# Kernel tuning notes

Measured on AMD Instinct MI355X. Metric: run time of the kernel, lower is better.

Reference implementation:

```python
import jax, jax.numpy as jnp
import numpy as np
import math

B, H, S, D = 2, 8, 2048, 64

def setup_inputs() -> dict:
    key = jax.random.key(0)
    kq, kk, kv, km = jax.random.split(key, 4)
    q = jax.random.normal(kq, (B, H, S, D), dtype=jnp.float32)
    k = jax.random.normal(kk, (B, H, S, D), dtype=jnp.float32)
    v = jax.random.normal(kv, (B, H, S, D), dtype=jnp.float32)
    mask = jax.random.randint(km, (B, S, S), 0, 2, dtype=jnp.int32)
    return {"q": q, "k": k, "v": v, "mask": mask}

def reference(q, k, v, mask):
    # NOTE: faithful to the torch module's quirks:
    #   d = k.size(1) -> scale by sqrt(n_heads), not sqrt(head_dim)
    #   softmax over dim=1 (the HEAD axis), not the key axis
    d = k.shape[1]
    # [B,H,S,S]
    att_score = jnp.einsum('bhqd,bhkd->bhqk', q, k) / math.sqrt(d)
    m = mask[:, None, :, :]  # unsqueeze(1) -> [B,1,S,S]
    att_score = jnp.where(m == 0, jnp.float32(-1e11), att_score)
    att_score = jax.nn.softmax(att_score, axis=1)  # softmax over head dim (quirk)
    # dropout is identity in eval mode
    z = jnp.einsum('bhqk,bhkd->bhqd', att_score, v)
    return (z, att_score)
```

## Files before the change

### kernel.cpp

```cpp
#include <hip/hip_runtime.h>
#include <hip/hip_bf16.h>
#include <cmath>

#define B_ 2
#define H_ 8
#define S_ 2048
#define D_ 64
#define TQ 16
#define TK 32
#define KCHUNKS 8
#define TPC ((S_ / TK) / KCHUNKS)

typedef __bf16 bf16x8 __attribute__((ext_vector_type(8)));
typedef float  f32x4  __attribute__((ext_vector_type(4)));

#define SB_STRIDE 33
#define AB_STRIDE 40


__global__ __launch_bounds__(256, 4)
void attn_fused(const float* __restrict__ qg, const float* __restrict__ kg,
                const float* __restrict__ vg, const int* __restrict__ maskg,
                float* __restrict__ zout, float* __restrict__ attout)
{
    __shared__ float  sbuf[H_][TQ][SB_STRIDE];
    __shared__ __bf16 abuf[H_][TQ][AB_STRIDE];

    const int tid  = threadIdx.x;
    const int lane = tid & 63;
    const int wave = tid >> 6;
    const int n16  = lane & 15;
    const int quad = lane >> 4;

    const int bi    = blockIdx.x;
    const int b     = bi & 1;
    const int qt    = (bi >> 1) & 127;
    const int chunk = bi >> 8;
    const int q0    = qt * TQ;

    const float scale = 0.35355339059327373f;

    bf16x8 qhi[2][2], qlo[2][2];
    #pragma unroll
    for (int hh = 0; hh < 2; ++hh) {
        const int h = wave * 2 + hh;
        const float* qp = qg + (size_t)((b * H_ + h) * S_ + q0 + n16) * D_;
        #pragma unroll
        for (int kk = 0; kk < 2; ++kk) {
            const float4* p = (const float4*)(qp + kk * 32 + quad * 8);
            float4 f0 = p[0], f1 = p[1];
            float fv[8] = {f0.x, f0.y, f0.z, f0.w, f1.x, f1.y, f1.z, f1.w};
            bf16x8 hi, lo;
            #pragma unroll
            for (int j = 0; j < 8; ++j) {
                float fs = fv[j] * scale;
                __bf16 h16 = (__bf16)fs;
                hi[j] = h16;
                lo[j] = (__bf16)(fs - (float)h16);
            }
            qhi[hh][kk] = hi; qlo[hh][kk] = lo;
        }
    }

    f32x4 acc[2][4];
    #pragma unroll
    for (int hh = 0; hh < 2; ++hh)
        #pragma unroll
        for (int d = 0; d < 4; ++d)
            acc[hh][d] = (f32x4){0.f, 0.f, 0.f, 0.f};

    for (int kt = 0; kt < TPC; ++kt) {
        const int k0 = chunk * (TK * TPC) + kt * TK;

        #pragma unroll
        for (int hh = 0; hh < 2; ++hh) {
            const int h = wave * 2 + hh;
            #pragma unroll
            for (int ks = 0; ks < 2; ++ks) {
                f32x4 c = (f32x4){0.f, 0.f, 0.f, 0.f};
                #pragma unroll
                for (int kk = 0; kk < 2; ++kk) {
                    const float* kp = kg + (size_t)((b * H_ + h) * S_ + k0 + ks * 16 + n16) * D_
                                      + kk * 32 + quad * 8;
                    float4 f0 = ((const float4*)kp)[0], f1 = ((const float4*)kp)[1];
                    float fv[8] = {f0.x, f0.y, f0.z, f0.w, f1.x, f1.y, f1.z, f1.w};
                    bf16x8 khi, klo;
                    #pragma unroll
                    for (int j = 0; j < 8; ++j) {
                        __bf16 h16 = (__bf16)fv[j];
                        khi[j] = h16;
                        klo[j] = (__bf16)(fv[j] - (float)h16);
                    }
                    c = __builtin_amdgcn_mfma_f32_16x16x32_bf16(qhi[hh][kk], khi, c, 0, 0, 0);
                    c = __builtin_amdgcn_mfma_f32_16x16x32_bf16(qlo[hh][kk], khi, c, 0, 0, 0);
                    c = __builtin_amdgcn_mfma_f32_16x16x32_bf16(qhi[hh][kk], klo, c, 0, 0, 0);
                }
                #pragma unroll
                for (int r = 0; r < 4; ++r)
                    sbuf[h][quad * 4 + r][ks * 16 + n16] = c[r];
            }
        }
        __syncthreads();

        #pragma unroll
        for (int rep = 0; rep < 2; ++rep) {
            const int pos = tid + rep * 256;
            const int qq  = pos >> 5;
            const int kk2 = pos & 31;
            const int msk = maskg[(size_t)(b * S_ + q0 + qq) * S_ + k0 + kk2];
            float sv[8];
            float mx = -INFINITY;
            #pragma unroll
            for (int h = 0; h < H_; ++h) { sv[h] = sbuf[h][qq][kk2]; mx = fmaxf(mx, sv[h]); }
            float sum = 0.f;
            #pragma unroll
            for (int h = 0; h < H_; ++h) { sv[h] = __expf(sv[h] - mx); sum += sv[h]; }
            const float inv = 1.0f / sum;
            #pragma unroll
            for (int h = 0; h < H_; ++h) {
                const float a = (msk == 0) ? 0.125f : sv[h] * inv;
                attout[(size_t)((b * H_ + h) * S_ + q0 + qq) * S_ + k0 + kk2] = a;
                abuf[h][qq][kk2] = (__bf16)a;
            }
        }
        __syncthreads();

        #pragma unroll
        for (int hh = 0; hh < 2; ++hh) {
            const int h = wave * 2 + hh;
            bf16x8 af = *(const bf16x8*)&abuf[h][n16][quad * 8];
            #pragma unroll
            for (int dsb = 0; dsb < 4; ++dsb) {
                const float* vp = vg + (size_t)((b * H_ + h) * S_ + k0 + quad * 8) * D_
                                  + dsb * 16 + n16;
                bf16x8 bf;
                #pragma unroll
                for (int j = 0; j < 8; ++j)
                    bf[j] = (__bf16)vp[(size_t)j * D_];
                acc[hh][dsb] = __builtin_amdgcn_mfma_f32_16x16x32_bf16(af, bf, acc[hh][dsb], 0, 0, 0);
            }
        }
    }

    #pragma unroll
    for (int hh = 0; hh < 2; ++hh) {
        const int h = wave * 2 + hh;
        #pragma unroll
        for (int dsb = 0; dsb < 4; ++dsb)
            #pragma unroll
            for (int r = 0; r < 4; ++r)
                atomicAdd(&zout[(size_t)((b * H_ + h) * S_ + q0 + quad * 4 + r) * D_
                                + dsb * 16 + n16],
                          acc[hh][dsb][r]);
    }
}

extern "C" void kernel_launch(void* const* d_in, const int* in_sizes, int n_in,
                              void* d_out, int out_size, void* d_ws, size_t ws_size,
                              hipStream_t stream) {
    const float* q    = (const float*)d_in[0];
    const float* k    = (const float*)d_in[1];
    const float* v    = (const float*)d_in[2];
    const int*   mask = (const int*)d_in[3];
    float* z   = (float*)d_out;
    float* att = (float*)d_out + (size_t)B_ * H_ * S_ * D_;

    hipMemsetAsync(z, 0, (size_t)B_ * H_ * S_ * D_ * sizeof(float), stream);

    attn_fused<<<dim3(KCHUNKS * B_ * (S_ / TQ)), dim3(256), 0, stream>>>(q, k, v, mask, z, att);
}
```

Measured before the change: 532.5 us.

## Precompute bf16 hi/lo K split and transposed bf16 V in prep kernels

Adds two preprocessing kernels. One splits K into bf16 hi/lo arrays once, so the main kernel no longer redoes the split for every query tile. The other writes V transposed in bf16, so the PV MFMA operand loads become one contiguous 16-byte read per lane instead of eight strided fp32 loads. The softmax phase now handles two keys per thread with vectorized mask, score, attention-output and abuf accesses, and the sbuf stride changes to match. This costs two extra launches and workspace traffic.

```diff
diff --git a/kernel.cpp b/kernel.cpp
--- a/kernel.cpp
+++ b/kernel.cpp
@@ -14,13 +14,66 @@
 typedef __bf16 bf16x8 __attribute__((ext_vector_type(8)));
 typedef float  f32x4  __attribute__((ext_vector_type(4)));
 
-#define SB_STRIDE 33
+#define SB_STRIDE 42
 #define AB_STRIDE 40
 
+#define NK ((size_t)B_ * H_ * S_ * D_)
+
+__global__ __launch_bounds__(256)
+void prep_k(const float* __restrict__ kg, __bf16* __restrict__ khi, __bf16* __restrict__ klo)
+{
+    const size_t i = ((size_t)blockIdx.x * 256 + threadIdx.x) * 8;
+    float4 f0 = ((const float4*)(kg + i))[0];
+    float4 f1 = ((const float4*)(kg + i))[1];
+    float fv[8] = {f0.x, f0.y, f0.z, f0.w, f1.x, f1.y, f1.z, f1.w};
+    bf16x8 hi, lo;
+    #pragma unroll
+    for (int j = 0; j < 8; ++j) {
+        __bf16 h = (__bf16)fv[j];
+        hi[j] = h;
+        lo[j] = (__bf16)(fv[j] - (float)h);
+    }
+    *(bf16x8*)(khi + i) = hi;
+    *(bf16x8*)(klo + i) = lo;
+}
+
+__global__ __launch_bounds__(256)
+void prep_vt(const float* __restrict__ vg, __bf16* __restrict__ vt)
+{
+    __shared__ float tile[64][65];
+    const int bh = blockIdx.x >> 5;
+    const int kt = blockIdx.x & 31;
+    const int t  = threadIdx.x;
+    {
+        const int key = t >> 2, seg = t & 3;
+        const float* src = vg + ((size_t)bh * S_ + kt * 64 + key) * D_ + seg * 16;
+        #pragma unroll
+        for (int i = 0; i < 4; ++i) {
+            float4 f = ((const float4*)src)[i];
+            tile[key][seg * 16 + i * 4 + 0] = f.x;
+            tile[key][seg * 16 + i * 4 + 1] = f.y;
+            tile[key][seg * 16 + i * 4 + 2] = f.z;
+            tile[key][seg * 16 + i * 4 + 3] = f.w;
+        }
+    }
+    __syncthreads();
+    {
+        const int d = t >> 2, seg = t & 3;
+        bf16x8 o0, o1;
+        #pragma unroll
+        for (int j = 0; j < 8; ++j) o0[j] = (__bf16)tile[seg * 16 + j][d];
+        #pragma unroll
+        for (int j = 0; j < 8; ++j) o1[j] = (__bf16)tile[seg * 16 + 8 + j][d];
+        __bf16* dst = vt + ((size_t)bh * D_ + d) * S_ + kt * 64 + seg * 16;
+        *(bf16x8*)dst       = o0;
+        *((bf16x8*)dst + 1) = o1;
+    }
+}
 
 __global__ __launch_bounds__(256, 4)
-void attn_fused(const float* __restrict__ qg, const float* __restrict__ kg,
-                const float* __restrict__ vg, const int* __restrict__ maskg,
+void attn_fused(const float* __restrict__ qg,
+                const __bf16* __restrict__ khi_g, const __bf16* __restrict__ klo_g,
+                const __bf16* __restrict__ vt_g,  const int* __restrict__ maskg,
                 float* __restrict__ zout, float* __restrict__ attout)
 {
     __shared__ float  sbuf[H_][TQ][SB_STRIDE];
@@ -69,6 +122,9 @@
         for (int d = 0; d < 4; ++d)
             acc[hh][d] = (f32x4){0.f, 0.f, 0.f, 0.f};
 
+    const int sqq = tid >> 4;
+    const int skp = (tid & 15) * 2;
+
     for (int kt = 0; kt < TPC; ++kt) {
         const int k0 = chunk * (TK * TPC) + kt * TK;
 
@@ -77,20 +133,13 @@
             const int h = wave * 2 + hh;
             #pragma unroll
             for (int ks = 0; ks < 2; ++ks) {
+                const size_t krow = ((size_t)(b * H_ + h) * S_ + k0 + ks * 16 + n16) * D_
+                                    + quad * 8;
                 f32x4 c = (f32x4){0.f, 0.f, 0.f, 0.f};
                 #pragma unroll
                 for (int kk = 0; kk < 2; ++kk) {
-                    const float* kp = kg + (size_t)((b * H_ + h) * S_ + k0 + ks * 16 + n16) * D_
-                                      + kk * 32 + quad * 8;
-                    float4 f0 = ((const float4*)kp)[0], f1 = ((const float4*)kp)[1];
-                    float fv[8] = {f0.x, f0.y, f0.z, f0.w, f1.x, f1.y, f1.z, f1.w};
-                    bf16x8 khi, klo;
-                    #pragma unroll
-                    for (int j = 0; j < 8; ++j) {
-                        __bf16 h16 = (__bf16)fv[j];
-                        khi[j] = h16;
-                        klo[j] = (__bf16)(fv[j] - (float)h16);
-                    }
+                    bf16x8 khi = *(const bf16x8*)(khi_g + krow + kk * 32);
+                    bf16x8 klo = *(const bf16x8*)(klo_g + krow + kk * 32);
                     c = __builtin_amdgcn_mfma_f32_16x16x32_bf16(qhi[hh][kk], khi, c, 0, 0, 0);
                     c = __builtin_amdgcn_mfma_f32_16x16x32_bf16(qlo[hh][kk], khi, c, 0, 0, 0);
                     c = __builtin_amdgcn_mfma_f32_16x16x32_bf16(qhi[hh][kk], klo, c, 0, 0, 0);
@@ -102,25 +151,32 @@
         }
         __syncthreads();
 
-        #pragma unroll
-        for (int rep = 0; rep < 2; ++rep) {
-            const int pos = tid + rep * 256;
-            const int qq  = pos >> 5;
-            const int kk2 = pos & 31;
-            const int msk = maskg[(size_t)(b * S_ + q0 + qq) * S_ + k0 + kk2];
-            float sv[8];
-            float mx = -INFINITY;
-            #pragma unroll
-            for (int h = 0; h < H_; ++h) { sv[h] = sbuf[h][qq][kk2]; mx = fmaxf(mx, sv[h]); }
-            float sum = 0.f;
-            #pragma unroll
-            for (int h = 0; h < H_; ++h) { sv[h] = __expf(sv[h] - mx); sum += sv[h]; }
-            const float inv = 1.0f / sum;
+        {
+            const int2 m2 = *(const int2*)&maskg[(size_t)(b * S_ + q0 + sqq) * S_ + k0 + skp];
+            float2 sv[8];
+            float mx0 = -INFINITY, mx1 = -INFINITY;
             #pragma unroll
             for (int h = 0; h < H_; ++h) {
-                const float a = (msk == 0) ? 0.125f : sv[h] * inv;
-                attout[(size_t)((b * H_ + h) * S_ + q0 + qq) * S_ + k0 + kk2] = a;
-                abuf[h][qq][kk2] = (__bf16)a;
+                float2 s = *(const float2*)&sbuf[h][sqq][skp];
+                sv[h] = s;
+                mx0 = fmaxf(mx0, s.x); mx1 = fmaxf(mx1, s.y);
+            }
+            float sum0 = 0.f, sum1 = 0.f;
+            #pragma unroll
+            for (int h = 0; h < H_; ++h) {
+                sv[h].x = __expf(sv[h].x - mx0); sum0 += sv[h].x;
+                sv[h].y = __expf(sv[h].y - mx1); sum1 += sv[h].y;
+            }
+            const float inv0 = 1.0f / sum0, inv1 = 1.0f / sum1;
+            #pragma unroll
+            for (int h = 0; h < H_; ++h) {
+                const float a0 = (m2.x == 0) ? 0.125f : sv[h].x * inv0;
+                const float a1 = (m2.y == 0) ? 0.125f : sv[h].y * inv1;
+                *(float2*)&attout[(size_t)((b * H_ + h) * S_ + q0 + sqq) * S_ + k0 + skp]
+                    = make_float2(a0, a1);
+                union { __bf16 bh2[2]; unsigned u; } pk;
+                pk.bh2[0] = (__bf16)a0; pk.bh2[1] = (__bf16)a1;
+                *(unsigned*)&abuf[h][sqq][skp] = pk.u;
             }
         }
         __syncthreads();
@@ -131,12 +187,8 @@
             bf16x8 af = *(const bf16x8*)&abuf[h][n16][quad * 8];
             #pragma unroll
             for (int dsb = 0; dsb < 4; ++dsb) {
-                const float* vp = vg + (size_t)((b * H_ + h) * S_ + k0 + quad * 8) * D_
-                                  + dsb * 16 + n16;
-                bf16x8 bf;
-                #pragma unroll
-                for (int j = 0; j < 8; ++j)
-                    bf[j] = (__bf16)vp[(size_t)j * D_];
+                bf16x8 bf = *(const bf16x8*)(vt_g
+                    + ((size_t)(b * H_ + h) * D_ + dsb * 16 + n16) * S_ + k0 + quad * 8);
                 acc[hh][dsb] = __builtin_amdgcn_mfma_f32_16x16x32_bf16(af, bf, acc[hh][dsb], 0, 0, 0);
             }
         }
@@ -163,9 +215,17 @@
     const float* v    = (const float*)d_in[2];
     const int*   mask = (const int*)d_in[3];
     float* z   = (float*)d_out;
-    float* att = (float*)d_out + (size_t)B_ * H_ * S_ * D_;
-
-    hipMemsetAsync(z, 0, (size_t)B_ * H_ * S_ * D_ * sizeof(float), stream);
-
-    attn_fused<<<dim3(KCHUNKS * B_ * (S_ / TQ)), dim3(256), 0, stream>>>(q, k, v, mask, z, att);
-}
+    float* att = (float*)d_out + NK;
+
+    __bf16* khi = (__bf16*)d_ws;
+    __bf16* klo = khi + NK;
+    __bf16* vt  = klo + NK;
+
+    prep_k <<<dim3(NK / (256 * 8)), dim3(256), 0, stream>>>(k, khi, klo);
+    prep_vt<<<dim3(B_ * H_ * (S_ / 64)), dim3(256), 0, stream>>>(v, vt);
+
+    hipMemsetAsync(z, 0, NK * sizeof(float), stream);
+
+    attn_fused<<<dim3(KCHUNKS * B_ * (S_ / TQ)), dim3(256), 0, stream>>>(
+        q, khi, klo, vt, mask, z, att);
+}
```

New measurement: 510.0 us. 1.04x faster.
